# Optimization experiments

Measured on AMD Instinct MI355X. Metric: run time of the kernel, lower is better.

Reference implementation:

```python
import jax, jax.numpy as jnp
import numpy as np
import math

EPS = 1e-5

def layernorm(x, w, b):
    mu = jnp.mean(x, axis=-1, keepdims=True)
    var = jnp.mean((x - mu) ** 2, axis=-1, keepdims=True)
    return (x - mu) / jnp.sqrt(var + EPS) * w + b

def pos_encoding(L, D):
    pos = jnp.arange(L, dtype=jnp.float32)[:, None]
    div = jnp.exp(jnp.arange(0, D, 2, dtype=jnp.float32) * (-math.log(10000.0) / D))
    pe = jnp.zeros((L, D), dtype=jnp.float32)
    pe = pe.at[:, 0::2].set(jnp.sin(pos * div))
    pe = pe.at[:, 1::2].set(jnp.cos(pos * div))
    return pe

def ssm_block(x, nw, nb, A, iw, ib, ow, ob):
    # x: [B,L,D]
    z = layernorm(x, nw, nb)
    proj = jnp.einsum('bld,ed->ble', z, iw) + ib  # [B,L,2D]
    u, g = jnp.split(proj, 2, axis=-1)
    g = jax.nn.sigmoid(g)
    u_t = jnp.swapaxes(u, 0, 1)  # [L,B,D]
    g_t = jnp.swapaxes(g, 0, 1)
    h0 = jnp.zeros(x.shape[::2], dtype=x.dtype)  # [B,D]
    def step(h, ug):
        ut, gt = ug
        h = gt * h + (1.0 - gt) * jnp.tanh(A * h + ut)
        return h, h
    _, hs = jax.lax.scan(step, h0, (u_t, g_t))  # hs: [L,B,D]
    out = jnp.einsum('lbd,ed->ble', hs, ow).swapaxes(0, 1).swapaxes(0, 1)
    out = jnp.einsum('lbd,ed->ble', hs, ow) + ob
    return x + out

def mha(x, qkv_w, qkv_b, ao_w, ao_b, nhead):
    B, L, D = x.shape
    dh = D // nhead
    qkv = jnp.einsum('bld,ed->ble', x, qkv_w) + qkv_b  # [B,L,3D]
    q, k, v = jnp.split(qkv, 3, axis=-1)
    def heads(t):
        return t.reshape(B, L, nhead, dh).transpose(0, 2, 1, 3)  # [B,H,L,dh]
    q, k, v = heads(q), heads(k), heads(v)
    scores = jnp.einsum('bhqd,bhkd->bhqk', q, k) / jnp.sqrt(jnp.asarray(dh, x.dtype))
    attn = jax.nn.softmax(scores, axis=-1)
    out = jnp.einsum('bhqk,bhkd->bhqd', attn, v)
    out = out.transpose(0, 2, 1, 3).reshape(B, L, D)
    return jnp.einsum('bld,ed->ble', out, ao_w) + ao_b

def encoder_layer(x, l1w, l1b, l2w, l2b, qkv_w, qkv_b, ao_w, ao_b, f1w, f1b, f2w, f2b, nhead):
    # norm_first pre-LN encoder layer, relu FFN, no dropout (eval)
    x = x + mha(layernorm(x, l1w, l1b), qkv_w, qkv_b, ao_w, ao_b, nhead)
    h = layernorm(x, l2w, l2b)
    h = jax.nn.relu(jnp.einsum('bld,fd->blf', h, f1w) + f1b)
    h = jnp.einsum('blf,df->bld', h, f2w) + f2b
    return x + h

def setup_inputs() -> dict:
    key = jax.random.key(0)
    ks = jax.random.split(key, 16)
    B, L, F, D, S, T = 8, 2048, 64, 128, 2, 2
    s = 0.05
    inp = {
        'x': jax.random.normal(ks[0], (B, L, F), jnp.float32),
        'in_w': jax.random.normal(ks[1], (D, F), jnp.float32) * s,
        'in_b': jnp.zeros((D,), jnp.float32),
        'ssm_norm_w': jnp.ones((S, D), jnp.float32),
        'ssm_norm_b': jnp.zeros((S, D), jnp.float32),
        'ssm_A': jax.random.normal(ks[2], (S, D), jnp.float32) * 0.1,
        'ssm_in_w': jax.random.normal(ks[3], (S, 2 * D, D), jnp.float32) * s,
        'ssm_in_b': jnp.zeros((S, 2 * D), jnp.float32),
        'ssm_out_w': jax.random.normal(ks[4], (S, D, D), jnp.float32) * s,
        'ssm_out_b': jnp.zeros((S, D), jnp.float32),
        'ln1_w': jnp.ones((T, D), jnp.float32),
        'ln1_b': jnp.zeros((T, D), jnp.float32),
        'ln2_w': jnp.ones((T, D), jnp.float32),
        'ln2_b': jnp.zeros((T, D), jnp.float32),
        'qkv_w': jax.random.normal(ks[5], (T, 3 * D, D), jnp.float32) * s,
        'qkv_b': jnp.zeros((T, 3 * D), jnp.float32),
        'ao_w': jax.random.normal(ks[6], (T, D, D), jnp.float32) * s,
        'ao_b': jnp.zeros((T, D), jnp.float32),
        'ff1_w': jax.random.normal(ks[7], (T, 4 * D, D), jnp.float32) * s,
        'ff1_b': jnp.zeros((T, 4 * D), jnp.float32),
        'ff2_w': jax.random.normal(ks[8], (T, D, 4 * D), jnp.float32) * s,
        'ff2_b': jnp.zeros((T, D), jnp.float32),
        'hln_w': jnp.ones((D,), jnp.float32),
        'hln_b': jnp.zeros((D,), jnp.float32),
        'h1_w': jax.random.normal(ks[9], (D, D), jnp.float32) * s,
        'h1_b': jnp.zeros((D,), jnp.float32),
        'h2_w': jax.random.normal(ks[10], (1, D), jnp.float32) * s,
        'h2_b': jnp.zeros((1,), jnp.float32),
    }
    return inp

NHEAD = 4

def reference(x, in_w, in_b, ssm_norm_w, ssm_norm_b, ssm_A, ssm_in_w, ssm_in_b,
              ssm_out_w, ssm_out_b, ln1_w, ln1_b, ln2_w, ln2_b, qkv_w, qkv_b,
              ao_w, ao_b, ff1_w, ff1_b, ff2_w, ff2_b, hln_w, hln_b, h1_w, h1_b,
              h2_w, h2_b):
    B, L, _ = x.shape
    D = in_w.shape[0]
    h = jnp.einsum('blf,df->bld', x, in_w) + in_b
    h = h + pos_encoding(L, D)[None]
    for i in range(ssm_A.shape[0]):
        h = ssm_block(h, ssm_norm_w[i], ssm_norm_b[i], ssm_A[i],
                      ssm_in_w[i], ssm_in_b[i], ssm_out_w[i], ssm_out_b[i])
    for i in range(ln1_w.shape[0]):
        h = encoder_layer(h, ln1_w[i], ln1_b[i], ln2_w[i], ln2_b[i],
                          qkv_w[i], qkv_b[i], ao_w[i], ao_b[i],
                          ff1_w[i], ff1_b[i], ff2_w[i], ff2_b[i], NHEAD)
    pooled = 0.5 * h[:, -1, :] + 0.5 * jnp.mean(h, axis=1)  # [B,D]
    p = layernorm(pooled, hln_w, hln_b)
    p = jax.nn.gelu(p @ h1_w.T + h1_b, approximate=False)
    return p @ h2_w.T + h2_b  # [B,1]
```

## Files before the change

kernel.cpp:

```cpp
#include <hip/hip_runtime.h>
#include <hip/hip_bf16.h>
#include <math.h>

#define L_SEQ 2048
#define D_MODEL 128
#define N_ROWS 16384
#define LOG2E 1.4426950408889634f

typedef __attribute__((ext_vector_type(8))) short bf16x8;
typedef __attribute__((ext_vector_type(4))) short short4v;
typedef __attribute__((ext_vector_type(4))) float f32x4;

__device__ __forceinline__ short f2bf(float x)
{
    __hip_bfloat16 b = __float2bfloat16(x);
    return *reinterpret_cast<short*>(&b);
}
__device__ __forceinline__ short f2bf_fast(float x)
{
    unsigned u = __builtin_bit_cast(unsigned, x);
    return (short)((u + 0x8000u) >> 16);
}
__device__ __forceinline__ float bf2f(short s)
{
    unsigned u = ((unsigned)(unsigned short)s) << 16;
    return __builtin_bit_cast(float, u);
}
__device__ __forceinline__ short f2h(float x)
{
    _Float16 h = (_Float16)x;
    return (short)__builtin_bit_cast(unsigned short, h);
}
__device__ __forceinline__ float h2f(short s)
{
    _Float16 h = __builtin_bit_cast(_Float16, (unsigned short)s);
    return (float)h;
}

__global__ __launch_bounds__(256) void convert_kernel(
    const float* __restrict__ x,    const float* __restrict__ inw,
    const float* __restrict__ ssmi, const float* __restrict__ ssmo,
    const float* __restrict__ qkvw, const float* __restrict__ aow,
    const float* __restrict__ f1w,  const float* __restrict__ f2w,
    short* __restrict__ xb, short* __restrict__ wb)
{
    int it = blockIdx.x * 256 + threadIdx.x;
    const float* src; short* dst; int off;
    if      (it < 131072) { src = x;    dst = xb;          off = it; }
    else if (it < 132096) { src = inw;  dst = wb;          off = it - 131072; }
    else if (it < 140288) { src = ssmi; dst = wb + 8192;   off = it - 132096; }
    else if (it < 144384) { src = ssmo; dst = wb + 73728;  off = it - 140288; }
    else if (it < 156672) { src = qkvw; dst = wb + 106496; off = it - 144384; }
    else if (it < 160768) { src = aow;  dst = wb + 204800; off = it - 156672; }
    else if (it < 177152) { src = f1w;  dst = wb + 237568; off = it - 160768; }
    else                  { src = f2w;  dst = wb + 368640; off = it - 177152; }
    off <<= 3;
    float4 v0 = *(const float4*)(src + off);
    float4 v1 = *(const float4*)(src + off + 4);
    bf16x8 p = {f2bf(v0.x), f2bf(v0.y), f2bf(v0.z), f2bf(v0.w),
                f2bf(v1.x), f2bf(v1.y), f2bf(v1.z), f2bf(v1.w)};
    *(bf16x8*)(dst + off) = p;
}

template <int FUSE>
__global__ __launch_bounds__(256) void gemm_ln(const short* __restrict__ A,
                                               const short* __restrict__ W,
                                               const float* __restrict__ bias,
                                               const float* __restrict__ lnw,
                                               const float* __restrict__ lnb,
                                               float* __restrict__ bh,
                                               short* __restrict__ lnout,
                                               int K)
{
    __shared__ __align__(16) short As[64][72];
    __shared__ __align__(16) short Bs[128][72];

    const int tid  = threadIdx.x;
    const int wave = tid >> 6;
    const int lane = tid & 63;
    const int m    = lane & 15;
    const int quad = lane >> 4;
    const int n0   = blockIdx.x * 64;

    const int arow = tid >> 2, acol = (tid & 3) << 4;
    const int brow = tid >> 1, bcol = (tid & 1) << 5;

    const short* Ap = A + (size_t)(n0 + arow) * K + acol;
    const short* Wp = W + (size_t)brow * K + bcol;

    f32x4 acc[8];
#pragma unroll
    for (int i = 0; i < 8; ++i) acc[i] = (f32x4){0.f, 0.f, 0.f, 0.f};

    bf16x8 a0 = *(const bf16x8*)Ap;
    bf16x8 a1 = *(const bf16x8*)(Ap + 8);
    bf16x8 b0 = *(const bf16x8*)Wp;
    bf16x8 b1 = *(const bf16x8*)(Wp + 8);
    bf16x8 b2 = *(const bf16x8*)(Wp + 16);
    bf16x8 b3 = *(const bf16x8*)(Wp + 24);

    for (int k0 = 0; k0 < K; k0 += 64) {
        *(bf16x8*)&As[arow][acol]      = a0;
        *(bf16x8*)&As[arow][acol + 8]  = a1;
        *(bf16x8*)&Bs[brow][bcol]      = b0;
        *(bf16x8*)&Bs[brow][bcol + 8]  = b1;
        *(bf16x8*)&Bs[brow][bcol + 16] = b2;
        *(bf16x8*)&Bs[brow][bcol + 24] = b3;
        __syncthreads();
        if (k0 + 64 < K) {
            a0 = *(const bf16x8*)(Ap + k0 + 64);
            a1 = *(const bf16x8*)(Ap + k0 + 72);
            b0 = *(const bf16x8*)(Wp + k0 + 64);
            b1 = *(const bf16x8*)(Wp + k0 + 72);
            b2 = *(const bf16x8*)(Wp + k0 + 80);
            b3 = *(const bf16x8*)(Wp + k0 + 88);
        }
#pragma unroll
        for (int ks = 0; ks < 2; ++ks) {
            bf16x8 af = *(const bf16x8*)&As[(wave << 4) + m][(ks << 5) + (quad << 3)];
#pragma unroll
            for (int nt = 0; nt < 8; ++nt) {
                bf16x8 bfr = *(const bf16x8*)&Bs[(nt << 4) + m][(ks << 5) + (quad << 3)];
                acc[nt] = __builtin_amdgcn_mfma_f32_16x16x32_bf16(af, bfr, acc[nt], 0, 0, 0);
            }
        }
        __syncthreads();
    }

#pragma unroll
    for (int nt = 0; nt < 8; ++nt) {
        int col = (nt << 4) + m;
        float bv = bias[col];
        float fr = 0.f;
        if (FUSE == 0)
            fr = __expf((float)(col & ~1) * (-0.07195578415606394f));
#pragma unroll
        for (int r = 0; r < 4; ++r) {
            int row = n0 + (wave << 4) + (quad << 2) + r;
            float t = acc[nt][r] + bv;
            if (FUSE == 0) {
                float ang = (float)(row & (L_SEQ - 1)) * fr;
                t += (col & 1) ? cosf(ang) : sinf(ang);
            } else {
                t += bh[(size_t)row * 128 + col];
            }
            acc[nt][r] = t;
            bh[(size_t)row * 128 + col] = t;
        }
    }

    if (FUSE < 2) {
        float wv[8], bvn[8];
#pragma unroll
        for (int nt = 0; nt < 8; ++nt) {
            wv[nt]  = lnw[(nt << 4) + m];
            bvn[nt] = lnb[(nt << 4) + m];
        }
#pragma unroll
        for (int r = 0; r < 4; ++r) {
            float s = 0.f;
#pragma unroll
            for (int nt = 0; nt < 8; ++nt) s += acc[nt][r];
            s += __shfl_xor(s, 1);
            s += __shfl_xor(s, 2);
            s += __shfl_xor(s, 4);
            s += __shfl_xor(s, 8);
            float mean = s * (1.f / 128.f);
            float q = 0.f;
#pragma unroll
            for (int nt = 0; nt < 8; ++nt) {
                float d = acc[nt][r] - mean;
                q = fmaf(d, d, q);
            }
            q += __shfl_xor(q, 1);
            q += __shfl_xor(q, 2);
            q += __shfl_xor(q, 4);
            q += __shfl_xor(q, 8);
            float inv = rsqrtf(q * (1.f / 128.f) + 1e-5f);
            int row = n0 + (wave << 4) + (quad << 2) + r;
#pragma unroll
            for (int nt = 0; nt < 8; ++nt) {
                int col = (nt << 4) + m;
                lnout[(size_t)row * 128 + col] =
                    f2bf((acc[nt][r] - mean) * inv * wv[nt] + bvn[nt]);
            }
        }
    }
}

enum { EPI_BF_RELU = 0, EPI_QKV = 1, EPI_SCAN_T = 2 };

template <int EPI>
__global__ __launch_bounds__(256) void gemm_bf(const short* __restrict__ A,
                                               const short* __restrict__ W,
                                               const float* __restrict__ bias,
                                               short* __restrict__ outb,
                                               short* __restrict__ outv,
                                               int K, int E)
{
    __shared__ __align__(16) short As[64][72];
    __shared__ __align__(16) short Bs[64][72];

    const int tid  = threadIdx.x;
    const int wave = tid >> 6;
    const int lane = tid & 63;
    const int m    = lane & 15;
    const int quad = lane >> 4;

    const int n0 = blockIdx.y * 64;
    const int e0 = blockIdx.x * 64;

    const int srow = tid >> 2;
    const int scol = (tid & 3) << 4;

    const short* Ap = A + (size_t)(n0 + srow) * K + scol;
    const short* Wp = W + (size_t)(e0 + srow) * K + scol;

    f32x4 acc[4];
#pragma unroll
    for (int i = 0; i < 4; ++i) acc[i] = (f32x4){0.f, 0.f, 0.f, 0.f};

    bf16x8 a0 = *(const bf16x8*)Ap;
    bf16x8 a1 = *(const bf16x8*)(Ap + 8);
    bf16x8 w0 = *(const bf16x8*)Wp;
    bf16x8 w1 = *(const bf16x8*)(Wp + 8);

    for (int k0 = 0; k0 < K; k0 += 64) {
        *(bf16x8*)&As[srow][scol]     = a0;
        *(bf16x8*)&As[srow][scol + 8] = a1;
        *(bf16x8*)&Bs[srow][scol]     = w0;
        *(bf16x8*)&Bs[srow][scol + 8] = w1;
        __syncthreads();
        if (k0 + 64 < K) {
            a0 = *(const bf16x8*)(Ap + k0 + 64);
            a1 = *(const bf16x8*)(Ap + k0 + 72);
            w0 = *(const bf16x8*)(Wp + k0 + 64);
            w1 = *(const bf16x8*)(Wp + k0 + 72);
        }
#pragma unroll
        for (int ks = 0; ks < 2; ++ks) {
            bf16x8 af = *(const bf16x8*)&As[(wave << 4) + m][(ks << 5) + (quad << 3)];
#pragma unroll
            for (int nt = 0; nt < 4; ++nt) {
                bf16x8 bfr = *(const bf16x8*)&Bs[(nt << 4) + m][(ks << 5) + (quad << 3)];
                acc[nt] = __builtin_amdgcn_mfma_f32_16x16x32_bf16(af, bfr, acc[nt], 0, 0, 0);
            }
        }
        __syncthreads();
    }

    if (EPI == EPI_QKV) {
        const float QSC = 0.17677669529663687f * LOG2E;
        if (e0 < 256) {
            short* dst = (e0 < 128) ? outb : (outb + 2097152);
            int cbase = (e0 < 128) ? e0 : (e0 - 128);
#pragma unroll
            for (int nt = 0; nt < 4; ++nt) {
                int col = cbase + (nt << 4) + m;
                float bv = bias[e0 + (nt << 4) + m];
#pragma unroll
                for (int r = 0; r < 4; ++r) {
                    int row = n0 + (wave << 4) + (quad << 2) + r;
                    float v = acc[nt][r] + bv;
                    if (e0 < 128) v *= QSC;
                    dst[(size_t)row * 128 + col] = f2bf(v);
                }
            }
        } else {
            int bb_ = n0 >> 11;
            int l0  = (n0 & (L_SEQ - 1)) + (wave << 4) + (quad << 2);
#pragma unroll
            for (int nt = 0; nt < 4; ++nt) {
                int c  = (e0 - 256) + (nt << 4) + m;
                int hh = c >> 5, dd = c & 31;
                float bv = bias[e0 + (nt << 4) + m];
                short4v pk;
#pragma unroll
                for (int r = 0; r < 4; ++r) pk[r] = f2bf(acc[nt][r] + bv);
                *(short4v*)&outv[(size_t)((bb_ * 4 + hh) * 32 + dd) * L_SEQ + l0] = pk;
            }
        }
    } else if (EPI == EPI_SCAN_T) {
        int bb_ = n0 >> 11;
        int l0  = (n0 & (L_SEQ - 1)) + (wave << 4) + (quad << 2);
#pragma unroll
        for (int nt = 0; nt < 4; ++nt) {
            int col = e0 + (nt << 4) + m;
            float bv = bias[col];
            short4v pk;
            if (e0 < 128) {
#pragma unroll
                for (int r = 0; r < 4; ++r)
                    pk[r] = f2h((acc[nt][r] + bv) * (2.f * LOG2E));
            } else {
#pragma unroll
                for (int r = 0; r < 4; ++r) {
                    float gr = acc[nt][r] + bv;
                    float g = __builtin_amdgcn_rcpf(
                        1.f + __builtin_amdgcn_exp2f(-gr * LOG2E));
                    pk[r] = f2h(g);
                }
            }
            *(short4v*)&outb[(((size_t)(bb_ * 256 + col)) << 11) + l0] = pk;
        }
    } else {
#pragma unroll
        for (int nt = 0; nt < 4; ++nt) {
            int col = e0 + (nt << 4) + m;
            float bv = bias[col];
#pragma unroll
            for (int r = 0; r < 4; ++r) {
                int row = n0 + (wave << 4) + (quad << 2) + r;
                float v = fmaxf(acc[nt][r] + bv, 0.f);
                outb[(size_t)row * E + col] = f2bf(v);
            }
        }
    }
}

#define SCAN_WARM 128

__device__ __forceinline__ void scan8(float& h, bf16x8 u8, bf16x8 g8,
                                      float a2, short* __restrict__ ob, int l0)
{
#pragma unroll
    for (int i = 0; i < 8; ++i) {
        float u2 = h2f(u8[i]);
        float g  = h2f(g8[i]);
        float omg = 1.f - g;
        float m2  = -2.f * omg;
        float c0 = fmaf(g, h, omg);
        float e2 = __builtin_amdgcn_exp2f(fmaf(a2, h, u2));
        float r  = __builtin_amdgcn_rcpf(1.f + e2);
        h = fmaf(m2, r, c0);
        ob[(l0 + i) * D_MODEL] = f2bf(h);
    }
}

__device__ __forceinline__ void scan8_ns(float& h, bf16x8 u8, bf16x8 g8,
                                         float a2)
{
#pragma unroll
    for (int i = 0; i < 8; ++i) {
        float u2 = h2f(u8[i]);
        float g  = h2f(g8[i]);
        float omg = 1.f - g;
        float m2  = -2.f * omg;
        float c0 = fmaf(g, h, omg);
        float e2 = __builtin_amdgcn_exp2f(fmaf(a2, h, u2));
        float r  = __builtin_amdgcn_rcpf(1.f + e2);
        h = fmaf(m2, r, c0);
    }
}

__global__ __launch_bounds__(64) void scan_kernel(const short* __restrict__ pt,
                                                  const float* __restrict__ A,
                                                  short* __restrict__ hs)
{
    int blk = blockIdx.x;
    int c   = blk & 15;
    int bd  = blk >> 4;
    int b   = bd >> 1;
    int d   = ((bd & 1) << 6) + threadIdx.x;
    float a2 = 2.f * A[d] * LOG2E;
    const short* up = pt + (((size_t)(b * 256 + d)) << 11);
    const short* gp = up + (((size_t)128) << 11);
    short* ob = hs + ((size_t)(b << 11)) * D_MODEL + d;

    const int lw = c << 7;
    float h = 0.f;

    bf16x8 uA0, uA1, gA0, gA1;

    if (c > 0) {
        int l0 = lw - SCAN_WARM;
        uA0 = *(const bf16x8*)(up + l0);
        uA1 = *(const bf16x8*)(up + l0 + 8);
        gA0 = *(const bf16x8*)(gp + l0);
        gA1 = *(const bf16x8*)(gp + l0 + 8);
        for (int l = l0; l < lw; l += 32) {
            bf16x8 uB0 = *(const bf16x8*)(up + l + 16);
            bf16x8 uB1 = *(const bf16x8*)(up + l + 24);
            bf16x8 gB0 = *(const bf16x8*)(gp + l + 16);
            bf16x8 gB1 = *(const bf16x8*)(gp + l + 24);
            scan8_ns(h, uA0, gA0, a2);
            scan8_ns(h, uA1, gA1, a2);
            uA0 = *(const bf16x8*)(up + l + 32);
            uA1 = *(const bf16x8*)(up + l + 40);
            gA0 = *(const bf16x8*)(gp + l + 32);
            gA1 = *(const bf16x8*)(gp + l + 40);
            scan8_ns(h, uB0, gB0, a2);
            scan8_ns(h, uB1, gB1, a2);
        }
    } else {
        uA0 = *(const bf16x8*)(up);
        uA1 = *(const bf16x8*)(up + 8);
        gA0 = *(const bf16x8*)(gp);
        gA1 = *(const bf16x8*)(gp + 8);
    }

    for (int l = lw; l < lw + 128; l += 32) {
        bf16x8 uB0 = *(const bf16x8*)(up + l + 16);
        bf16x8 uB1 = *(const bf16x8*)(up + l + 24);
        bf16x8 gB0 = *(const bf16x8*)(gp + l + 16);
        bf16x8 gB1 = *(const bf16x8*)(gp + l + 24);
        scan8(h, uA0, gA0, a2, ob, l);
        scan8(h, uA1, gA1, a2, ob, l + 8);
        if (l + 32 < lw + 128) {
            uA0 = *(const bf16x8*)(up + l + 32);
            uA1 = *(const bf16x8*)(up + l + 40);
            gA0 = *(const bf16x8*)(gp + l + 32);
            gA1 = *(const bf16x8*)(gp + l + 40);
        }
        scan8(h, uB0, gB0, a2, ob, l + 16);
        scan8(h, uB1, gB1, a2, ob, l + 24);
    }
}

__global__ __launch_bounds__(256) void attn_kernel(const short* __restrict__ Qs,
                                                   const short* __restrict__ Ks,
                                                   const short* __restrict__ Vtg,
                                                   short* __restrict__ outb)
{
    __shared__ __align__(16) short Klds[2][64][40];
    __shared__ __align__(16) short Vlds[2][32][72];
    __shared__ __align__(16) short Plds[4][16][72];

    const int tid  = threadIdx.x;
    const int wave = tid >> 6;
    const int lane = tid & 63;
    const int m    = lane & 15;
    const int quad = lane >> 4;

    const int raw = blockIdx.x;
    const int bid = (raw & 7) * 128 + (raw >> 3);
    const int b  = bid >> 7;
    const int h  = (bid >> 5) & 3;
    const int q0 = (bid & 31) << 6;

    bf16x8 qfrag = *(const bf16x8*)&Qs[((size_t)((b << 11) + q0 + (wave << 4) + m)) * 128
                                       + (h << 5) + (quad << 3)];

    f32x4 O[2];
    O[0] = (f32x4){0.f, 0.f, 0.f, 0.f};
    O[1] = (f32x4){0.f, 0.f, 0.f, 0.f};
    float rs = 0.f;

    const int krow = tid >> 2, dg = (tid & 3) << 3;
    const int vrow = tid >> 3, kg = (tid & 7) << 3;
    const short* kbase = Ks + ((size_t)(b << 11) + krow) * 128 + (h << 5) + dg;
    const short* vbase = Vtg + ((size_t)((b << 2) + h) * 32 + vrow) * L_SEQ + kg;

    bf16x8 kreg = *(const bf16x8*)kbase;
    bf16x8 vreg = *(const bf16x8*)vbase;
    *(bf16x8*)&Klds[0][krow][dg] = kreg;
    *(bf16x8*)&Vlds[0][vrow][kg] = vreg;
    __syncthreads();

    for (int kc = 0; kc < 32; ++kc) {
        const int cur = kc & 1;
        if (kc < 31) {
            kreg = *(const bf16x8*)(kbase + (size_t)((kc + 1) << 6) * 128);
            vreg = *(const bf16x8*)(vbase + ((kc + 1) << 6));
        }

#pragma unroll
        for (int kt = 0; kt < 4; ++kt) {
            bf16x8 kf = *(const bf16x8*)&Klds[cur][(kt << 4) + m][quad << 3];
            f32x4 S = __builtin_amdgcn_mfma_f32_16x16x32_bf16(
                kf, qfrag, (f32x4){0.f, 0.f, 0.f, 0.f}, 0, 0, 0);
            short4v pk;
#pragma unroll
            for (int r = 0; r < 4; ++r) {
                float p = __builtin_amdgcn_exp2f(S[r]);
                rs += p;
                pk[r] = f2bf_fast(p);
            }
            *(short4v*)&Plds[wave][m][(kt << 4) + (quad << 2)] = pk;
        }

#pragma unroll
        for (int kt2 = 0; kt2 < 2; ++kt2) {
            bf16x8 pf = *(const bf16x8*)&Plds[wave][m][(kt2 << 5) + (quad << 3)];
#pragma unroll
            for (int dt = 0; dt < 2; ++dt) {
                bf16x8 vf = *(const bf16x8*)&Vlds[cur][(dt << 4) + m][(kt2 << 5) + (quad << 3)];
                O[dt] = __builtin_amdgcn_mfma_f32_16x16x32_bf16(pf, vf, O[dt], 0, 0, 0);
            }
        }

        if (kc < 31) {
            *(bf16x8*)&Klds[cur ^ 1][krow][dg] = kreg;
            *(bf16x8*)&Vlds[cur ^ 1][vrow][kg] = vreg;
        }
        __syncthreads();
    }

    rs += __shfl_xor(rs, 16);
    rs += __shfl_xor(rs, 32);

#pragma unroll
    for (int r = 0; r < 4; ++r) {
        float sv  = __shfl(rs, (quad << 2) + r);
        float inv = 1.f / sv;
        int row = (b << 11) + q0 + (wave << 4) + (quad << 2) + r;
        short* op = outb + (size_t)row * D_MODEL + (h << 5) + m;
        op[0]  = f2bf(O[0][r] * inv);
        op[16] = f2bf(O[1][r] * inv);
    }
}

__global__ __launch_bounds__(1024) void pool_head_kernel(
    const float* __restrict__ h,
    const float* __restrict__ hlnw, const float* __restrict__ hlnb,
    const float* __restrict__ h1w, const float* __restrict__ h1b,
    const float* __restrict__ h2w, const float* __restrict__ h2b,
    float* __restrict__ out)
{
    __shared__ float part[8][128];
    __shared__ float sd[128];
    __shared__ float sq[128];

    int b   = blockIdx.x;
    int t   = threadIdx.x;
    int d   = t & 127;
    int seg = t >> 7;
    const float* hb = h + (size_t)b * L_SEQ * D_MODEL;

    float acc = 0.f;
    int l0 = seg << 8;
    for (int l = l0; l < l0 + 256; l += 4) {
        acc += hb[(l + 0) * D_MODEL + d] + hb[(l + 1) * D_MODEL + d]
             + hb[(l + 2) * D_MODEL + d] + hb[(l + 3) * D_MODEL + d];
    }
    part[seg][d] = acc;
    __syncthreads();

    float v = 0.f;
    if (t < 128) {
        float s = 0.f;
#pragma unroll
        for (int i = 0; i < 8; ++i) s += part[i][t];
        v = 0.5f * hb[(L_SEQ - 1) * D_MODEL + t] + 0.5f * (s * (1.f / (float)L_SEQ));
        sd[t] = v;
    }
    __syncthreads();
    for (int s = 64; s > 0; s >>= 1) {
        if (t < s) sd[t] += sd[t + s];
        __syncthreads();
    }
    float mu = sd[0] * (1.f / 128.f);
    __syncthreads();
    float dv = v - mu;
    if (t < 128) sd[t] = dv * dv;
    __syncthreads();
    for (int s = 64; s > 0; s >>= 1) {
        if (t < s) sd[t] += sd[t + s];
        __syncthreads();
    }
    float var = sd[0] * (1.f / 128.f);
    __syncthreads();
    if (t < 128) sq[t] = dv * rsqrtf(var + 1e-5f) * hlnw[t] + hlnb[t];
    __syncthreads();
    if (t < 128) {
        float dot = h1b[t];
        for (int d2 = 0; d2 < 128; ++d2) dot = fmaf(sq[d2], h1w[t * 128 + d2], dot);
        float ge = 0.5f * dot * (1.f + erff(dot * 0.7071067811865475f));
        sd[t] = ge * h2w[t];
    }
    __syncthreads();
    for (int s = 64; s > 0; s >>= 1) {
        if (t < s) sd[t] += sd[t + s];
        __syncthreads();
    }
    if (t == 0) out[b] = sd[0] + h2b[0];
}

extern "C" void kernel_launch(void* const* d_in, const int* in_sizes, int n_in,
                              void* d_out, int out_size, void* d_ws, size_t ws_size,
                              hipStream_t stream)
{
    (void)in_sizes; (void)n_in; (void)out_size; (void)ws_size;
    const float* x      = (const float*)d_in[0];
    const float* in_w   = (const float*)d_in[1];
    const float* in_b   = (const float*)d_in[2];
    const float* ssm_nw = (const float*)d_in[3];
    const float* ssm_nb = (const float*)d_in[4];
    const float* ssm_A  = (const float*)d_in[5];
    const float* ssm_iw = (const float*)d_in[6];
    const float* ssm_ib = (const float*)d_in[7];
    const float* ssm_ow = (const float*)d_in[8];
    const float* ssm_ob = (const float*)d_in[9];
    const float* ln1w   = (const float*)d_in[10];
    const float* ln1b   = (const float*)d_in[11];
    const float* ln2w   = (const float*)d_in[12];
    const float* ln2b   = (const float*)d_in[13];
    const float* qkvw   = (const float*)d_in[14];
    const float* qkvb   = (const float*)d_in[15];
    const float* aow    = (const float*)d_in[16];
    const float* aob    = (const float*)d_in[17];
    const float* f1w    = (const float*)d_in[18];
    const float* f1b    = (const float*)d_in[19];
    const float* f2w    = (const float*)d_in[20];
    const float* f2b    = (const float*)d_in[21];
    const float* hlnw   = (const float*)d_in[22];
    const float* hlnb   = (const float*)d_in[23];
    const float* h1w    = (const float*)d_in[24];
    const float* h1b    = (const float*)d_in[25];
    const float* h2w    = (const float*)d_in[26];
    const float* h2b    = (const float*)d_in[27];
    float* out = (float*)d_out;

    char* wsb = (char*)d_ws;
    float* bh     = (float*)(wsb);
    short* abuf   = (short*)(wsb + 8388608);
    short* bbuf   = (short*)(wsb + 25165824);
    short* qs     = (short*)(wsb + 29360128);
    short* vt     = (short*)(wsb + 37748736);
    short* xb     = (short*)(wsb + 41943040);
    short* wb     = (short*)(wsb + 44040192);
    short* ks     = qs + 2097152;

    dim3 blk(256);

    convert_kernel<<<756, blk, 0, stream>>>(x, in_w, ssm_iw, ssm_ow, qkvw, aow, f1w, f2w, xb, wb);

    gemm_ln<0><<<256, blk, 0, stream>>>(
        xb, wb, in_b, ssm_nw, ssm_nb, bh, bbuf, 64);

    gemm_bf<EPI_SCAN_T><<<dim3(4, 256), blk, 0, stream>>>(
        bbuf, wb + 8192, ssm_ib, abuf, nullptr, 128, 256);
    scan_kernel<<<256, 64, 0, stream>>>(abuf, ssm_A, bbuf);
    gemm_ln<1><<<256, blk, 0, stream>>>(
        bbuf, wb + 73728, ssm_ob, ssm_nw + 128, ssm_nb + 128, bh, bbuf, 128);

    gemm_bf<EPI_SCAN_T><<<dim3(4, 256), blk, 0, stream>>>(
        bbuf, wb + 8192 + 32768, ssm_ib + 256, abuf, nullptr, 128, 256);
    scan_kernel<<<256, 64, 0, stream>>>(abuf, ssm_A + 128, bbuf);
    gemm_ln<1><<<256, blk, 0, stream>>>(
        bbuf, wb + 73728 + 16384, ssm_ob + 128, ln1w, ln1b, bh, bbuf, 128);

    gemm_bf<EPI_QKV><<<dim3(6, 256), blk, 0, stream>>>(
        bbuf, wb + 106496, qkvb, qs, vt, 128, 384);
    attn_kernel<<<1024, blk, 0, stream>>>(qs, ks, vt, bbuf);
    gemm_ln<1><<<256, blk, 0, stream>>>(
        bbuf, wb + 204800, aob, ln2w, ln2b, bh, bbuf, 128);
    gemm_bf<EPI_BF_RELU><<<dim3(8, 256), blk, 0, stream>>>(
        bbuf, wb + 237568, f1b, abuf, nullptr, 128, 512);
    gemm_ln<1><<<256, blk, 0, stream>>>(
        abuf, wb + 368640, f2b, ln1w + 128, ln1b + 128, bh, bbuf, 512);

    gemm_bf<EPI_QKV><<<dim3(6, 256), blk, 0, stream>>>(
        bbuf, wb + 106496 + 49152, qkvb + 384, qs, vt, 128, 384);
    attn_kernel<<<1024, blk, 0, stream>>>(qs, ks, vt, bbuf);
    gemm_ln<1><<<256, blk, 0, stream>>>(
        bbuf, wb + 204800 + 16384, aob + 128, ln2w + 128, ln2b + 128, bh, bbuf, 128);
    gemm_bf<EPI_BF_RELU><<<dim3(8, 256), blk, 0, stream>>>(
        bbuf, wb + 237568 + 65536, f1b + 512, abuf, nullptr, 128, 512);
    gemm_ln<2><<<256, blk, 0, stream>>>(
        abuf, wb + 368640 + 65536, f2b + 128, nullptr, nullptr, bh, nullptr, 512);

    pool_head_kernel<<<8, 1024, 0, stream>>>(bh, hlnw, hlnb, h1w, h1b, h2w, h2b, out);
}
```

Baseline: 356.3 us.

## Halve gemm_ln row tile with cross-wave LN reduction; pack bf16 conversion in attention

```diff
diff --git a/kernel.cpp b/kernel.cpp
--- a/kernel.cpp
+++ b/kernel.cpp
@@ -20,6 +20,12 @@
 {
     unsigned u = __builtin_bit_cast(unsigned, x);
     return (short)((u + 0x8000u) >> 16);
+}
+__device__ __forceinline__ unsigned cvt_pk_bf16(float lo, float hi)
+{
+    unsigned r;
+    asm("v_cvt_pk_bf16_f32 %0, %1, %2" : "=v"(r) : "v"(lo), "v"(hi));
+    return r;
 }
 __device__ __forceinline__ float bf2f(short s)
 {
@@ -72,28 +78,30 @@
                                                short* __restrict__ lnout,
                                                int K)
 {
-    __shared__ __align__(16) short As[64][72];
+    __shared__ __align__(16) short As[32][72];
     __shared__ __align__(16) short Bs[128][72];
+    __shared__ float2 red[2][32];
 
     const int tid  = threadIdx.x;
     const int wave = tid >> 6;
     const int lane = tid & 63;
     const int m    = lane & 15;
     const int quad = lane >> 4;
-    const int n0   = blockIdx.x * 64;
-
-    const int arow = tid >> 2, acol = (tid & 3) << 4;
+    const int rh   = wave & 1;
+    const int ch   = wave >> 1;
+    const int n0   = blockIdx.x * 32;
+
+    const int arow = tid >> 3, acol = (tid & 7) << 3;
     const int brow = tid >> 1, bcol = (tid & 1) << 5;
 
     const short* Ap = A + (size_t)(n0 + arow) * K + acol;
     const short* Wp = W + (size_t)brow * K + bcol;
 
-    f32x4 acc[8];
-#pragma unroll
-    for (int i = 0; i < 8; ++i) acc[i] = (f32x4){0.f, 0.f, 0.f, 0.f};
+    f32x4 acc[4];
+#pragma unroll
+    for (int i = 0; i < 4; ++i) acc[i] = (f32x4){0.f, 0.f, 0.f, 0.f};
 
     bf16x8 a0 = *(const bf16x8*)Ap;
-    bf16x8 a1 = *(const bf16x8*)(Ap + 8);
     bf16x8 b0 = *(const bf16x8*)Wp;
     bf16x8 b1 = *(const bf16x8*)(Wp + 8);
     bf16x8 b2 = *(const bf16x8*)(Wp + 16);
@@ -101,7 +109,6 @@
 
     for (int k0 = 0; k0 < K; k0 += 64) {
         *(bf16x8*)&As[arow][acol]      = a0;
-        *(bf16x8*)&As[arow][acol + 8]  = a1;
         *(bf16x8*)&Bs[brow][bcol]      = b0;
         *(bf16x8*)&Bs[brow][bcol + 8]  = b1;
         *(bf16x8*)&Bs[brow][bcol + 16] = b2;
@@ -109,7 +116,6 @@
         __syncthreads();
         if (k0 + 64 < K) {
             a0 = *(const bf16x8*)(Ap + k0 + 64);
-            a1 = *(const bf16x8*)(Ap + k0 + 72);
             b0 = *(const bf16x8*)(Wp + k0 + 64);
             b1 = *(const bf16x8*)(Wp + k0 + 72);
             b2 = *(const bf16x8*)(Wp + k0 + 80);
@@ -117,10 +123,10 @@
         }
 #pragma unroll
         for (int ks = 0; ks < 2; ++ks) {
-            bf16x8 af = *(const bf16x8*)&As[(wave << 4) + m][(ks << 5) + (quad << 3)];
-#pragma unroll
-            for (int nt = 0; nt < 8; ++nt) {
-                bf16x8 bfr = *(const bf16x8*)&Bs[(nt << 4) + m][(ks << 5) + (quad << 3)];
+            bf16x8 af = *(const bf16x8*)&As[(rh << 4) + m][(ks << 5) + (quad << 3)];
+#pragma unroll
+            for (int nt = 0; nt < 4; ++nt) {
+                bf16x8 bfr = *(const bf16x8*)&Bs[(ch << 6) + (nt << 4) + m][(ks << 5) + (quad << 3)];
                 acc[nt] = __builtin_amdgcn_mfma_f32_16x16x32_bf16(af, bfr, acc[nt], 0, 0, 0);
             }
         }
@@ -128,15 +134,15 @@
     }
 
 #pragma unroll
-    for (int nt = 0; nt < 8; ++nt) {
-        int col = (nt << 4) + m;
+    for (int nt = 0; nt < 4; ++nt) {
+        int col = (ch << 6) + (nt << 4) + m;
         float bv = bias[col];
         float fr = 0.f;
         if (FUSE == 0)
             fr = __expf((float)(col & ~1) * (-0.07195578415606394f));
 #pragma unroll
         for (int r = 0; r < 4; ++r) {
-            int row = n0 + (wave << 4) + (quad << 2) + r;
+            int row = n0 + (rh << 4) + (quad << 2) + r;
             float t = acc[nt][r] + bv;
             if (FUSE == 0) {
                 float ang = (float)(row & (L_SEQ - 1)) * fr;
@@ -150,37 +156,42 @@
     }
 
     if (FUSE < 2) {
-        float wv[8], bvn[8];
-#pragma unroll
-        for (int nt = 0; nt < 8; ++nt) {
-            wv[nt]  = lnw[(nt << 4) + m];
-            bvn[nt] = lnb[(nt << 4) + m];
-        }
+        float wv[4], bvn[4];
+#pragma unroll
+        for (int nt = 0; nt < 4; ++nt) {
+            wv[nt]  = lnw[(ch << 6) + (nt << 4) + m];
+            bvn[nt] = lnb[(ch << 6) + (nt << 4) + m];
+        }
+        float s1[4], s2[4];
 #pragma unroll
         for (int r = 0; r < 4; ++r) {
-            float s = 0.f;
-#pragma unroll
-            for (int nt = 0; nt < 8; ++nt) s += acc[nt][r];
-            s += __shfl_xor(s, 1);
-            s += __shfl_xor(s, 2);
-            s += __shfl_xor(s, 4);
-            s += __shfl_xor(s, 8);
-            float mean = s * (1.f / 128.f);
-            float q = 0.f;
-#pragma unroll
-            for (int nt = 0; nt < 8; ++nt) {
-                float d = acc[nt][r] - mean;
-                q = fmaf(d, d, q);
-            }
-            q += __shfl_xor(q, 1);
-            q += __shfl_xor(q, 2);
-            q += __shfl_xor(q, 4);
-            q += __shfl_xor(q, 8);
-            float inv = rsqrtf(q * (1.f / 128.f) + 1e-5f);
-            int row = n0 + (wave << 4) + (quad << 2) + r;
-#pragma unroll
-            for (int nt = 0; nt < 8; ++nt) {
-                int col = (nt << 4) + m;
+            float s = 0.f, q = 0.f;
+#pragma unroll
+            for (int nt = 0; nt < 4; ++nt) {
+                float t = acc[nt][r];
+                s += t;
+                q = fmaf(t, t, q);
+            }
+            s += __shfl_xor(s, 1);  q += __shfl_xor(q, 1);
+            s += __shfl_xor(s, 2);  q += __shfl_xor(q, 2);
+            s += __shfl_xor(s, 4);  q += __shfl_xor(q, 4);
+            s += __shfl_xor(s, 8);  q += __shfl_xor(q, 8);
+            s1[r] = s; s2[r] = q;
+            if (m == 0) red[ch][(rh << 4) + (quad << 2) + r] = make_float2(s, q);
+        }
+        __syncthreads();
+#pragma unroll
+        for (int r = 0; r < 4; ++r) {
+            float2 o = red[ch ^ 1][(rh << 4) + (quad << 2) + r];
+            float ts = s1[r] + o.x;
+            float tq = s2[r] + o.y;
+            float mean = ts * (1.f / 128.f);
+            float var  = tq * (1.f / 128.f) - mean * mean;
+            float inv  = rsqrtf(var + 1e-5f);
+            int row = n0 + (rh << 4) + (quad << 2) + r;
+#pragma unroll
+            for (int nt = 0; nt < 4; ++nt) {
+                int col = (ch << 6) + (nt << 4) + m;
                 lnout[(size_t)row * 128 + col] =
                     f2bf((acc[nt][r] - mean) * inv * wv[nt] + bvn[nt]);
             }
@@ -424,7 +435,7 @@
 {
     __shared__ __align__(16) short Klds[2][64][40];
     __shared__ __align__(16) short Vlds[2][32][72];
-    __shared__ __align__(16) short Plds[4][16][72];
+    __shared__ __align__(16) short Plds[4][16][68];
 
     const int tid  = threadIdx.x;
     const int wave = tid >> 6;
@@ -469,19 +480,23 @@
             bf16x8 kf = *(const bf16x8*)&Klds[cur][(kt << 4) + m][quad << 3];
             f32x4 S = __builtin_amdgcn_mfma_f32_16x16x32_bf16(
                 kf, qfrag, (f32x4){0.f, 0.f, 0.f, 0.f}, 0, 0, 0);
-            short4v pk;
-#pragma unroll
-            for (int r = 0; r < 4; ++r) {
-                float p = __builtin_amdgcn_exp2f(S[r]);
-                rs += p;
-                pk[r] = f2bf_fast(p);
-            }
-            *(short4v*)&Plds[wave][m][(kt << 4) + (quad << 2)] = pk;
+            float p0 = __builtin_amdgcn_exp2f(S[0]);
+            float p1 = __builtin_amdgcn_exp2f(S[1]);
+            float p2 = __builtin_amdgcn_exp2f(S[2]);
+            float p3 = __builtin_amdgcn_exp2f(S[3]);
+            rs += p0 + p1 + p2 + p3;
+            uint2 pk;
+            pk.x = cvt_pk_bf16(p0, p1);
+            pk.y = cvt_pk_bf16(p2, p3);
+            *(uint2*)&Plds[wave][m][(kt << 4) + (quad << 2)] = pk;
         }
 
 #pragma unroll
         for (int kt2 = 0; kt2 < 2; ++kt2) {
-            bf16x8 pf = *(const bf16x8*)&Plds[wave][m][(kt2 << 5) + (quad << 3)];
+            short4v plo = *(const short4v*)&Plds[wave][m][(kt2 << 5) + (quad << 3)];
+            short4v phi = *(const short4v*)&Plds[wave][m][(kt2 << 5) + (quad << 3) + 4];
+            bf16x8 pf = {plo[0], plo[1], plo[2], plo[3],
+                         phi[0], phi[1], phi[2], phi[3]};
 #pragma unroll
             for (int dt = 0; dt < 2; ++dt) {
                 bf16x8 vf = *(const bf16x8*)&Vlds[cur][(dt << 4) + m][(kt2 << 5) + (quad << 3)];
@@ -625,39 +640,39 @@
 
     convert_kernel<<<756, blk, 0, stream>>>(x, in_w, ssm_iw, ssm_ow, qkvw, aow, f1w, f2w, xb, wb);
 
-    gemm_ln<0><<<256, blk, 0, stream>>>(
+    gemm_ln<0><<<512, blk, 0, stream>>>(
         xb, wb, in_b, ssm_nw, ssm_nb, bh, bbuf, 64);
 
     gemm_bf<EPI_SCAN_T><<<dim3(4, 256), blk, 0, stream>>>(
         bbuf, wb + 8192, ssm_ib, abuf, nullptr, 128, 256);
     scan_kernel<<<256, 64, 0, stream>>>(abuf, ssm_A, bbuf);
-    gemm_ln<1><<<256, blk, 0, stream>>>(
+    gemm_ln<1><<<512, blk, 0, stream>>>(
         bbuf, wb + 73728, ssm_ob, ssm_nw + 128, ssm_nb + 128, bh, bbuf, 128);
 
     gemm_bf<EPI_SCAN_T><<<dim3(4, 256), blk, 0, stream>>>(
         bbuf, wb + 8192 + 32768, ssm_ib + 256, abuf, nullptr, 128, 256);
     scan_kernel<<<256, 64, 0, stream>>>(abuf, ssm_A + 128, bbuf);
-    gemm_ln<1><<<256, blk, 0, stream>>>(
+    gemm_ln<1><<<512, blk, 0, stream>>>(
         bbuf, wb + 73728 + 16384, ssm_ob + 128, ln1w, ln1b, bh, bbuf, 128);
 
     gemm_bf<EPI_QKV><<<dim3(6, 256), blk, 0, stream>>>(
         bbuf, wb + 106496, qkvb, qs, vt, 128, 384);
     attn_kernel<<<1024, blk, 0, stream>>>(qs, ks, vt, bbuf);
-    gemm_ln<1><<<256, blk, 0, stream>>>(
+    gemm_ln<1><<<512, blk, 0, stream>>>(
         bbuf, wb + 204800, aob, ln2w, ln2b, bh, bbuf, 128);
     gemm_bf<EPI_BF_RELU><<<dim3(8, 256), blk, 0, stream>>>(
         bbuf, wb + 237568, f1b, abuf, nullptr, 128, 512);
-    gemm_ln<1><<<256, blk, 0, stream>>>(
+    gemm_ln<1><<<512, blk, 0, stream>>>(
         abuf, wb + 368640, f2b, ln1w + 128, ln1b + 128, bh, bbuf, 512);
 
     gemm_bf<EPI_QKV><<<dim3(6, 256), blk, 0, stream>>>(
         bbuf, wb + 106496 + 49152, qkvb + 384, qs, vt, 128, 384);
     attn_kernel<<<1024, blk, 0, stream>>>(qs, ks, vt, bbuf);
-    gemm_ln<1><<<256, blk, 0, stream>>>(
+    gemm_ln<1><<<512, blk, 0, stream>>>(
         bbuf, wb + 204800 + 16384, aob + 128, ln2w + 128, ln2b + 128, bh, bbuf, 128);
     gemm_bf<EPI_BF_RELU><<<dim3(8, 256), blk, 0, stream>>>(
         bbuf, wb + 237568 + 65536, f1b + 512, abuf, nullptr, 128, 512);
-    gemm_ln<2><<<256, blk, 0, stream>>>(
+    gemm_ln<2><<<512, blk, 0, stream>>>(
         abuf, wb + 368640 + 65536, f2b + 128, nullptr, nullptr, bh, nullptr, 512);
 
     pool_head_kernel<<<8, 1024, 0, stream>>>(bh, hlnw, hlnb, h1w, h1b, h2w, h2b, out);
```

After: 347.4 us. -2.5%, faster.
